# Kernel tuning notes

Hardware: AMD Instinct MI355X
Metric: run time of the kernel (lower is better)

Reference implementation:

```python
import jax, jax.numpy as jnp
import numpy as np

B, P, D, C = 1024, 4, 512, 128  # batch, parts, feat_dim, num_classes


def setup_inputs() -> dict:
    key = jax.random.key(0)
    k1, k2 = jax.random.split(key)
    # scale 0.05 keeps dot products O(1) so exp() stays in fp32 range
    inputs = jax.random.normal(k1, (B, P, D), dtype=jnp.float32) * 0.05
    targets = jax.random.randint(k2, (B,), 0, C, dtype=jnp.int64)
    return {"inputs": inputs, "targets": targets}


def _npairs_loss(inputs, targets):
    b, p, d = inputs.shape
    n = b * p
    X = inputs.reshape(n, d)
    t = jnp.repeat(targets, p)              # (n,) class label per row
    parts = jnp.tile(jnp.arange(p), b)      # (n,) part id per row
    prod = X @ X.T                          # (n, n) similarities

    sc = t[:, None] == t[None, :]           # same class
    sp = parts[:, None] == parts[None, :]   # same attention part
    s_sadc = (~sc) & sp
    s_dasc = sc & (~sp)
    s_dadc = (~sc) & (~sp)

    e_pos = jnp.exp(prod)                   # exp(neg) terms
    e_neg = jnp.exp(-prod)                  # exp(-pos) terms

    def group_loss(pos_mask, neg_mask):
        # sum_i sum_{j in pos_i} log(1 + sum_{k in neg_i} exp(prod[i,k] - prod[i,j]))
        # = sum log1p(S_i * exp(-prod[i,j])) with S_i = sum_{k in neg_i} exp(prod[i,k])
        S = jnp.sum(jnp.where(neg_mask, e_pos, 0.0), axis=1)        # (n,)
        terms = jnp.where(pos_mask, jnp.log1p(S[:, None] * e_neg), 0.0)
        return jnp.sum(terms)

    loss_sadc = group_loss(s_sadc, s_dadc)
    loss_dasc = group_loss(s_dasc, s_dadc)
    # NOTE: original returns loss_sadc twice and never uses loss_sasc (bug kept for fidelity)
    return (loss_sadc + loss_sadc + loss_dasc) / n


def reference(inputs, targets):
    return _npairs_loss(inputs, targets)
```

## Files before the change

### kernel.cpp

```cpp
#include <hip/hip_runtime.h>
#include <stdint.h>

#define GLOBAL_AS __attribute__((address_space(1)))
#define LDS_AS    __attribute__((address_space(3)))

typedef __attribute__((ext_vector_type(8))) __bf16 bf16x8;
typedef __attribute__((ext_vector_type(4))) float  f32x4;

static_assert(sizeof(bf16x8) == 16, "bf16x8 must be 16B");

constexpr int N  = 4096;
constexpr int DK = 512;
constexpr int NTILE = 528;
constexpr int PW = 32;


__global__ void k_convert(const float* __restrict__ X, __bf16* __restrict__ Xb,
                          const int* __restrict__ tbuf, int* __restrict__ cls) {
    if (blockIdx.x == 1024) {
        __shared__ int is64;
        const int t = threadIdx.x;
        if (t == 0) is64 = 1;
        __syncthreads();
        if (tbuf[4 * t + 1] != 0 || tbuf[4 * t + 3] != 0) is64 = 0;
        __syncthreads();
        const int f = is64;
#pragma unroll
        for (int q = 0; q < 4; ++q) {
            const int ti = 4 * t + q;
            const int v = tbuf[f ? 2 * ti : ti];
            cls[4 * ti + 0] = v; cls[4 * ti + 1] = v;
            cls[4 * ti + 2] = v; cls[4 * ti + 3] = v;
        }
        return;
    }
    int idx = blockIdx.x * blockDim.x + threadIdx.x;
    const float4* s = (const float4*)X;
    float4 a = s[2 * idx + 0];
    float4 b = s[2 * idx + 1];
    bf16x8 o;
    o[0] = (__bf16)a.x; o[1] = (__bf16)a.y; o[2] = (__bf16)a.z; o[3] = (__bf16)a.w;
    o[4] = (__bf16)b.x; o[5] = (__bf16)b.y; o[6] = (__bf16)b.z; o[7] = (__bf16)b.w;
    *(bf16x8*)(Xb + 8 * idx) = o;
}

__launch_bounds__(256, 3)
__global__ void k_main(const __bf16* __restrict__ Xb, const int* __restrict__ cls,
                       float* __restrict__ partials) {
    __shared__ __align__(16) char smem[3][16384];
    __shared__ int rowcls[128], colcls[128];
    float4* accR = (float4*)&smem[0][0];
    float4* accC = (float4*)&smem[1][0];

    const int tid  = threadIdx.x;
    const int lane = tid & 63;
    const int wid  = tid >> 6;
    const int wr   = wid >> 1;
    const int wc   = wid & 1;
    const int rA   = lane & 15;
    const int kgrp = lane >> 4;
    const char* xb = (const char*)Xb;

    const int bid = (blockIdx.x & 7) * 66 + (blockIdx.x >> 3);
    int rt = (int)((sqrtf(8.0f * (float)bid + 1.0f) - 1.0f) * 0.5f);
    while (((rt + 1) * (rt + 2)) / 2 <= bid) ++rt;
    while ((rt * (rt + 1)) / 2 > bid) --rt;
    const int g  = bid - (rt * (rt + 1)) / 2;
    const int i0 = rt * 128;
    const int j0 = g * 128;
    const bool offdiag = (rt != g);

    if (tid < 128) rowcls[tid] = cls[i0 + tid];
    else           colcls[tid - 128] = cls[j0 + (tid - 128)];
    __syncthreads();

    size_t gbase[4];
#pragma unroll
    for (int q = 0; q < 4; ++q) {
        const int l    = q * 256 + tid;
        const int prow = l >> 2;
        const int csrc = (l & 3) ^ ((prow >> 1) & 3);
        const int grow = (prow < 128) ? (i0 + prow) : (j0 + prow - 128);
        gbase[q] = (size_t)grow * 1024 + (size_t)(csrc * 16);
    }

#define STAGE(bslot, kt)                                                       \
    {                                                                          \
        char* dst = &smem[(bslot)][0];                                         \
        const size_t kb = (size_t)(kt) * 64;                                   \
        _Pragma("unroll")                                                      \
        for (int q = 0; q < 4; ++q) {                                          \
            __builtin_amdgcn_global_load_lds(                                  \
                (const GLOBAL_AS void*)(xb + gbase[q] + kb),                   \
                (LDS_AS void*)(dst + q * 4096 + wid * 1024), 16, 0, 0);        \
        }                                                                      \
    }

    STAGE(0, 0);
    STAGE(1, 1);

    f32x4 acc[4][4] = {};

#pragma unroll
    for (int t = 0; t < 16; ++t) {
        if (t < 15) { asm volatile("s_waitcnt vmcnt(4)" ::: "memory"); }
        else        { asm volatile("s_waitcnt vmcnt(0)" ::: "memory"); }
        __builtin_amdgcn_s_barrier();
        asm volatile("" ::: "memory");
        if (t + 2 < 16) STAGE((t + 2) % 3, t + 2);
        const char* bp = &smem[t % 3][0];
        bf16x8 af[4], bg[4];
#pragma unroll
        for (int m = 0; m < 4; ++m) {
            const int pr = wr * 64 + m * 16 + rA;
            af[m] = *(const bf16x8*)(bp + pr * 64 + ((kgrp ^ ((pr >> 1) & 3)) << 4));
        }
#pragma unroll
        for (int n = 0; n < 4; ++n) {
            const int pr = 128 + wc * 64 + n * 16 + rA;
            bg[n] = *(const bf16x8*)(bp + pr * 64 + ((kgrp ^ ((pr >> 1) & 3)) << 4));
        }
#pragma unroll
        for (int m = 0; m < 4; ++m)
#pragma unroll
            for (int n = 0; n < 4; ++n)
                acc[m][n] = __builtin_amdgcn_mfma_f32_16x16x32_bf16(bg[n], af[m],
                                                                    acc[m][n], 0, 0, 0);
    }
#undef STAGE

    __syncthreads();

    const int pi = rA & 3;
    int ci[4];
#pragma unroll
    for (int m = 0; m < 4; ++m) ci[m] = rowcls[wr * 64 + m * 16 + rA];
    float rS[4] = {0.f, 0.f, 0.f, 0.f};
    float rP[4] = {0.f, 0.f, 0.f, 0.f};
    float rE[4] = {0.f, 0.f, 0.f, 0.f};
    float rW[4] = {0.f, 0.f, 0.f, 0.f};

#pragma unroll
    for (int n = 0; n < 4; ++n) {
#pragma unroll
        for (int r = 0; r < 4; ++r) {
            const int cj = colcls[wc * 64 + n * 16 + kgrp * 4 + r];
            float cS = 0.f, cP = 0.f, cE = 0.f, cW = 0.f;
#pragma unroll
            for (int m = 0; m < 4; ++m) {
                const float p  = acc[m][n][r];
                const float ep = __expf(p);
                const bool sc = (ci[m] == cj);
                const bool sp = (pi == r);
                if (!sc && !sp) { rS[m] += ep; cS += ep; }
                const float w = (!sc && sp) ? 2.f : ((sc && !sp) ? 1.f : 0.f);
                rP[m] += w * p;  rE[m] += w * ep;  rW[m] += w;
                cP += w * p;     cE += w * ep;     cW += w;
            }
            if (offdiag) {
#pragma unroll
                for (int off = 1; off < 16; off <<= 1) {
                    cS += __shfl_xor(cS, off);
                    cP += __shfl_xor(cP, off);
                    cE += __shfl_xor(cE, off);
                    cW += __shfl_xor(cW, off);
                }
                if (rA == 0)
                    accC[wr * 128 + wc * 64 + n * 16 + kgrp * 4 + r] =
                        make_float4(cS, cP, cE, cW);
            }
        }
    }
#pragma unroll
    for (int m = 0; m < 4; ++m) {
        float vS = rS[m], vP = rP[m], vE = rE[m], vW = rW[m];
        vS += __shfl_xor(vS, 16); vS += __shfl_xor(vS, 32);
        vP += __shfl_xor(vP, 16); vP += __shfl_xor(vP, 32);
        vE += __shfl_xor(vE, 16); vE += __shfl_xor(vE, 32);
        vW += __shfl_xor(vW, 16); vW += __shfl_xor(vW, 32);
        if (kgrp == 0) accR[wc * 128 + wr * 64 + m * 16 + rA] = make_float4(vS, vP, vE, vW);
    }

    __syncthreads();
    if (tid < 128) {
        float4 a0 = accR[tid], a1 = accR[128 + tid];
        ((float4*)partials)[(size_t)(i0 + tid) * PW + g] =
            make_float4(a0.x + a1.x, a0.y + a1.y, a0.z + a1.z, a0.w + a1.w);
    } else if (offdiag) {
        const int c = tid - 128;
        float4 c0 = accC[c], c1 = accC[128 + c];
        ((float4*)partials)[(size_t)(j0 + c) * PW + rt] =
            make_float4(c0.x + c1.x, c0.y + c1.y, c0.z + c1.z, c0.w + c1.w);
    }
}

__global__ void k_rowloss(const float* __restrict__ partials, float* __restrict__ blockSums) {
    __shared__ float red[16];
    const int tid = threadIdx.x;
    const int sub = tid & 15;
    const int row = blockIdx.x * 16 + (tid >> 4);

    const float4* p = ((const float4*)partials) + (size_t)row * PW;
    float4 a = p[sub];
    float4 b = p[sub + 16];
    float S = a.x + b.x, P = a.y + b.y, E = a.z + b.z, W = a.w + b.w;
#pragma unroll
    for (int off = 1; off < 16; off <<= 1) {
        S += __shfl_xor(S, off);
        P += __shfl_xor(P, off);
        E += __shfl_xor(E, off);
        W += __shfl_xor(W, off);
    }
    if (sub == 0) red[tid >> 4] = W * logf(S) - P + E / S;
    __syncthreads();
    if (tid == 0) {
        float s = 0.f;
#pragma unroll
        for (int r = 0; r < 16; ++r) s += red[r];
        blockSums[blockIdx.x] = s;
    }
}

__global__ void k_final2(const float* __restrict__ blockSums, float* __restrict__ out) {
    const int t = threadIdx.x;
    float v = blockSums[t] + blockSums[t + 64] + blockSums[t + 128] + blockSums[t + 192];
#pragma unroll
    for (int off = 1; off < 64; off <<= 1) v += __shfl_xor(v, off);
    if (t == 0) out[0] = v / (float)N;
}

extern "C" void kernel_launch(void* const* d_in, const int* in_sizes, int n_in,
                              void* d_out, int out_size, void* d_ws, size_t ws_size,
                              hipStream_t stream) {
    const float* X = (const float*)d_in[0];
    const int*   T = (const int*)d_in[1];
    float* out = (float*)d_out;

    char* ws = (char*)d_ws;
    __bf16* Xb    = (__bf16*)ws;
    int*    cls   = (int*)(ws + (size_t)4 * 1024 * 1024);
    float*  parts = (float*)(ws + (size_t)4 * 1024 * 1024 + 16 * 1024);
    float*  bsums = (float*)ws;

    hipLaunchKernelGGL(k_convert, dim3(1025),  dim3(256), 0, stream, X, Xb, T, cls);
    hipLaunchKernelGGL(k_main,    dim3(NTILE), dim3(256), 0, stream, Xb, cls, parts);
    hipLaunchKernelGGL(k_rowloss, dim3(256),   dim3(256), 0, stream, parts, bsums);
    hipLaunchKernelGGL(k_final2,  dim3(1),     dim3(64),  0, stream, bsums, out);
}
```

Measured before the change: 57.03 us.

## Switch Gram matrix GEMM from bf16 to fp8 MFMA and transpose partials layout

Inputs are converted to fp8 (e4m3) instead of bf16, halving the bytes staged per row, and the main kernel uses 16x16x32 fp8 MFMAs over 8 K-tiles instead of 16 bf16 tiles. The LDS swizzle and fragment loads are adapted to 8-byte fp8 operands. The partials buffer is transposed to slot-major so the row-loss kernel uses one thread per row with 16 blocks, and the final reduce is shrunk to match. Precision loss from fp8 on the dot products, which feed exp(), may push the loss outside tolerance.

```diff
diff --git a/kernel.cpp b/kernel.cpp
--- a/kernel.cpp
+++ b/kernel.cpp
@@ -4,10 +4,7 @@
 #define GLOBAL_AS __attribute__((address_space(1)))
 #define LDS_AS    __attribute__((address_space(3)))
 
-typedef __attribute__((ext_vector_type(8))) __bf16 bf16x8;
-typedef __attribute__((ext_vector_type(4))) float  f32x4;
-
-static_assert(sizeof(bf16x8) == 16, "bf16x8 must be 16B");
+typedef __attribute__((ext_vector_type(4))) float f32x4;
 
 constexpr int N  = 4096;
 constexpr int DK = 512;
@@ -15,7 +12,7 @@
 constexpr int PW = 32;
 
 
-__global__ void k_convert(const float* __restrict__ X, __bf16* __restrict__ Xb,
+__global__ void k_convert(const float* __restrict__ X, uint32_t* __restrict__ Xb8,
                           const int* __restrict__ tbuf, int* __restrict__ cls) {
     if (blockIdx.x == 1024) {
         __shared__ int is64;
@@ -34,18 +31,21 @@
         }
         return;
     }
-    int idx = blockIdx.x * blockDim.x + threadIdx.x;
+    const int idx = blockIdx.x * blockDim.x + threadIdx.x;
     const float4* s = (const float4*)X;
     float4 a = s[2 * idx + 0];
     float4 b = s[2 * idx + 1];
-    bf16x8 o;
-    o[0] = (__bf16)a.x; o[1] = (__bf16)a.y; o[2] = (__bf16)a.z; o[3] = (__bf16)a.w;
-    o[4] = (__bf16)b.x; o[5] = (__bf16)b.y; o[6] = (__bf16)b.z; o[7] = (__bf16)b.w;
-    *(bf16x8*)(Xb + 8 * idx) = o;
+    uint32_t lo = 0, hi = 0;
+    lo = __builtin_amdgcn_cvt_pk_fp8_f32(a.x, a.y, lo, 0);
+    lo = __builtin_amdgcn_cvt_pk_fp8_f32(a.z, a.w, lo, 1);
+    hi = __builtin_amdgcn_cvt_pk_fp8_f32(b.x, b.y, hi, 0);
+    hi = __builtin_amdgcn_cvt_pk_fp8_f32(b.z, b.w, hi, 1);
+    Xb8[2 * idx + 0] = lo;
+    Xb8[2 * idx + 1] = hi;
 }
 
 __launch_bounds__(256, 3)
-__global__ void k_main(const __bf16* __restrict__ Xb, const int* __restrict__ cls,
+__global__ void k_main(const char* __restrict__ Xb, const int* __restrict__ cls,
                        float* __restrict__ partials) {
     __shared__ __align__(16) char smem[3][16384];
     __shared__ int rowcls[128], colcls[128];
@@ -59,7 +59,6 @@
     const int wc   = wid & 1;
     const int rA   = lane & 15;
     const int kgrp = lane >> 4;
-    const char* xb = (const char*)Xb;
 
     const int bid = (blockIdx.x & 7) * 66 + (blockIdx.x >> 3);
     int rt = (int)((sqrtf(8.0f * (float)bid + 1.0f) - 1.0f) * 0.5f);
@@ -79,9 +78,9 @@
     for (int q = 0; q < 4; ++q) {
         const int l    = q * 256 + tid;
         const int prow = l >> 2;
-        const int csrc = (l & 3) ^ ((prow >> 1) & 3);
+        const int csrc = (l & 3) ^ (prow & 3);
         const int grow = (prow < 128) ? (i0 + prow) : (j0 + prow - 128);
-        gbase[q] = (size_t)grow * 1024 + (size_t)(csrc * 16);
+        gbase[q] = (size_t)grow * DK + (size_t)(csrc * 16);
     }
 
 #define STAGE(bslot, kt)                                                       \
@@ -91,7 +90,7 @@
         _Pragma("unroll")                                                      \
         for (int q = 0; q < 4; ++q) {                                          \
             __builtin_amdgcn_global_load_lds(                                  \
-                (const GLOBAL_AS void*)(xb + gbase[q] + kb),                   \
+                (const GLOBAL_AS void*)(Xb + gbase[q] + kb),                   \
                 (LDS_AS void*)(dst + q * 4096 + wid * 1024), 16, 0, 0);        \
         }                                                                      \
     }
@@ -102,30 +101,35 @@
     f32x4 acc[4][4] = {};
 
 #pragma unroll
-    for (int t = 0; t < 16; ++t) {
-        if (t < 15) { asm volatile("s_waitcnt vmcnt(4)" ::: "memory"); }
-        else        { asm volatile("s_waitcnt vmcnt(0)" ::: "memory"); }
+    for (int t = 0; t < 8; ++t) {
+        if (t < 7) { asm volatile("s_waitcnt vmcnt(4)" ::: "memory"); }
+        else       { asm volatile("s_waitcnt vmcnt(0)" ::: "memory"); }
         __builtin_amdgcn_s_barrier();
         asm volatile("" ::: "memory");
-        if (t + 2 < 16) STAGE((t + 2) % 3, t + 2);
+        if (t + 2 < 8) STAGE((t + 2) % 3, t + 2);
         const char* bp = &smem[t % 3][0];
-        bf16x8 af[4], bg[4];
-#pragma unroll
-        for (int m = 0; m < 4; ++m) {
-            const int pr = wr * 64 + m * 16 + rA;
-            af[m] = *(const bf16x8*)(bp + pr * 64 + ((kgrp ^ ((pr >> 1) & 3)) << 4));
+#pragma unroll
+        for (int kk = 0; kk < 2; ++kk) {
+            long af[4], bg[4];
+            const int c  = kk * 2 + (kgrp >> 1);
+            const int s8 = (kgrp & 1) * 8;
+#pragma unroll
+            for (int m = 0; m < 4; ++m) {
+                const int pr = wr * 64 + m * 16 + rA;
+                af[m] = *(const long*)(bp + pr * 64 + ((c ^ (pr & 3)) << 4) + s8);
+            }
+#pragma unroll
+            for (int n = 0; n < 4; ++n) {
+                const int pr = 128 + wc * 64 + n * 16 + rA;
+                bg[n] = *(const long*)(bp + pr * 64 + ((c ^ (pr & 3)) << 4) + s8);
+            }
+#pragma unroll
+            for (int m = 0; m < 4; ++m)
+#pragma unroll
+                for (int n = 0; n < 4; ++n)
+                    acc[m][n] = __builtin_amdgcn_mfma_f32_16x16x32_fp8_fp8(
+                        bg[n], af[m], acc[m][n], 0, 0, 0);
         }
-#pragma unroll
-        for (int n = 0; n < 4; ++n) {
-            const int pr = 128 + wc * 64 + n * 16 + rA;
-            bg[n] = *(const bf16x8*)(bp + pr * 64 + ((kgrp ^ ((pr >> 1) & 3)) << 4));
-        }
-#pragma unroll
-        for (int m = 0; m < 4; ++m)
-#pragma unroll
-            for (int n = 0; n < 4; ++n)
-                acc[m][n] = __builtin_amdgcn_mfma_f32_16x16x32_bf16(bg[n], af[m],
-                                                                    acc[m][n], 0, 0, 0);
     }
 #undef STAGE
 
@@ -184,48 +188,41 @@
     __syncthreads();
     if (tid < 128) {
         float4 a0 = accR[tid], a1 = accR[128 + tid];
-        ((float4*)partials)[(size_t)(i0 + tid) * PW + g] =
+        ((float4*)partials)[(size_t)g * N + i0 + tid] =
             make_float4(a0.x + a1.x, a0.y + a1.y, a0.z + a1.z, a0.w + a1.w);
     } else if (offdiag) {
         const int c = tid - 128;
         float4 c0 = accC[c], c1 = accC[128 + c];
-        ((float4*)partials)[(size_t)(j0 + c) * PW + rt] =
+        ((float4*)partials)[(size_t)rt * N + j0 + c] =
             make_float4(c0.x + c1.x, c0.y + c1.y, c0.z + c1.z, c0.w + c1.w);
     }
 }
 
 __global__ void k_rowloss(const float* __restrict__ partials, float* __restrict__ blockSums) {
-    __shared__ float red[16];
+    __shared__ float red[256];
     const int tid = threadIdx.x;
-    const int sub = tid & 15;
-    const int row = blockIdx.x * 16 + (tid >> 4);
-
-    const float4* p = ((const float4*)partials) + (size_t)row * PW;
-    float4 a = p[sub];
-    float4 b = p[sub + 16];
-    float S = a.x + b.x, P = a.y + b.y, E = a.z + b.z, W = a.w + b.w;
-#pragma unroll
-    for (int off = 1; off < 16; off <<= 1) {
-        S += __shfl_xor(S, off);
-        P += __shfl_xor(P, off);
-        E += __shfl_xor(E, off);
-        W += __shfl_xor(W, off);
-    }
-    if (sub == 0) red[tid >> 4] = W * logf(S) - P + E / S;
-    __syncthreads();
-    if (tid == 0) {
-        float s = 0.f;
-#pragma unroll
-        for (int r = 0; r < 16; ++r) s += red[r];
-        blockSums[blockIdx.x] = s;
-    }
+    const int row = blockIdx.x * 256 + tid;
+    const float4* p = (const float4*)partials;
+    float S = 0.f, P = 0.f, E = 0.f, W = 0.f;
+#pragma unroll
+    for (int s = 0; s < PW; ++s) {
+        float4 v = p[(size_t)s * N + row];
+        S += v.x; P += v.y; E += v.z; W += v.w;
+    }
+    red[tid] = W * logf(S) - P + E / S;
+    __syncthreads();
+    for (int s = 128; s > 0; s >>= 1) {
+        if (tid < s) red[tid] += red[tid + s];
+        __syncthreads();
+    }
+    if (tid == 0) blockSums[blockIdx.x] = red[0];
 }
 
 __global__ void k_final2(const float* __restrict__ blockSums, float* __restrict__ out) {
     const int t = threadIdx.x;
-    float v = blockSums[t] + blockSums[t + 64] + blockSums[t + 128] + blockSums[t + 192];
-#pragma unroll
-    for (int off = 1; off < 64; off <<= 1) v += __shfl_xor(v, off);
+    float v = (t < 16) ? blockSums[t] : 0.f;
+#pragma unroll
+    for (int off = 1; off < 16; off <<= 1) v += __shfl_xor(v, off);
     if (t == 0) out[0] = v / (float)N;
 }
 
@@ -237,13 +234,14 @@
     float* out = (float*)d_out;
 
     char* ws = (char*)d_ws;
-    __bf16* Xb    = (__bf16*)ws;
-    int*    cls   = (int*)(ws + (size_t)4 * 1024 * 1024);
-    float*  parts = (float*)(ws + (size_t)4 * 1024 * 1024 + 16 * 1024);
-    float*  bsums = (float*)ws;
-
-    hipLaunchKernelGGL(k_convert, dim3(1025),  dim3(256), 0, stream, X, Xb, T, cls);
-    hipLaunchKernelGGL(k_main,    dim3(NTILE), dim3(256), 0, stream, Xb, cls, parts);
-    hipLaunchKernelGGL(k_rowloss, dim3(256),   dim3(256), 0, stream, parts, bsums);
+    char*     Xb8   = ws;
+    int*      cls   = (int*)(ws + (size_t)2 * 1024 * 1024);
+    float*    parts = (float*)(ws + (size_t)2 * 1024 * 1024 + 16 * 1024);
+    float*    bsums = (float*)ws;
+
+    hipLaunchKernelGGL(k_convert, dim3(1025),  dim3(256), 0, stream,
+                       X, (uint32_t*)Xb8, T, cls);
+    hipLaunchKernelGGL(k_main,    dim3(NTILE), dim3(256), 0, stream, Xb8, cls, parts);
+    hipLaunchKernelGGL(k_rowloss, dim3(16),    dim3(256), 0, stream, parts, bsums);
     hipLaunchKernelGGL(k_final2,  dim3(1),     dim3(64),  0, stream, bsums, out);
 }
```

Result: slower. 61.30 us (+7.5%).

## Use 512-thread blocks with 8 waves and double-buffered LDS staging in k_main

Applied to the files above, without the earlier changes.

Doubles the block to 8 wavefronts arranged 2x4, so each wave computes a 64x32 sub-tile instead of 64x64, with correspondingly fewer accumulators per wave. The three-stage LDS ring with explicit vmcnt waits becomes a two-buffer ping-pong synchronised by __syncthreads, and the epilogue reduces four row partials instead of two. The aim is more resident waves to hide latency and lower register pressure. In exchange it gives up prefetch depth and per-wave operand reuse, and the tighter launch-bounds occupancy hint could force register spills.

```diff
diff --git a/kernel.cpp b/kernel.cpp
--- a/kernel.cpp
+++ b/kernel.cpp
@@ -12,7 +12,6 @@
 constexpr int N  = 4096;
 constexpr int DK = 512;
 constexpr int NTILE = 528;
-constexpr int PW = 32;
 
 
 __global__ void k_convert(const float* __restrict__ X, __bf16* __restrict__ Xb,
@@ -44,10 +43,10 @@
     *(bf16x8*)(Xb + 8 * idx) = o;
 }
 
-__launch_bounds__(256, 3)
+__launch_bounds__(512, 6)
 __global__ void k_main(const __bf16* __restrict__ Xb, const int* __restrict__ cls,
                        float* __restrict__ partials) {
-    __shared__ __align__(16) char smem[3][16384];
+    __shared__ __align__(16) char smem[2][16384];
     __shared__ int rowcls[128], colcls[128];
     float4* accR = (float4*)&smem[0][0];
     float4* accC = (float4*)&smem[1][0];
@@ -55,8 +54,8 @@
     const int tid  = threadIdx.x;
     const int lane = tid & 63;
     const int wid  = tid >> 6;
-    const int wr   = wid >> 1;
-    const int wc   = wid & 1;
+    const int wr   = wid >> 2;
+    const int wc   = wid & 3;
     const int rA   = lane & 15;
     const int kgrp = lane >> 4;
     const char* xb = (const char*)Xb;
@@ -70,62 +69,63 @@
     const int j0 = g * 128;
     const bool offdiag = (rt != g);
 
-    if (tid < 128) rowcls[tid] = cls[i0 + tid];
-    else           colcls[tid - 128] = cls[j0 + (tid - 128)];
-    __syncthreads();
-
-    size_t gbase[4];
-#pragma unroll
-    for (int q = 0; q < 4; ++q) {
-        const int l    = q * 256 + tid;
+    if (tid < 128) {
+        rowcls[tid] = cls[i0 + tid];
+        colcls[tid] = cls[j0 + tid];
+    }
+
+    size_t gbase[2];
+#pragma unroll
+    for (int q = 0; q < 2; ++q) {
+        const int l    = q * 512 + tid;
         const int prow = l >> 2;
         const int csrc = (l & 3) ^ ((prow >> 1) & 3);
         const int grow = (prow < 128) ? (i0 + prow) : (j0 + prow - 128);
         gbase[q] = (size_t)grow * 1024 + (size_t)(csrc * 16);
     }
 
-#define STAGE(bslot, kt)                                                       \
+#define STAGE(buf, kt)                                                         \
     {                                                                          \
-        char* dst = &smem[(bslot)][0];                                         \
+        char* dst = &smem[(buf)][0];                                           \
         const size_t kb = (size_t)(kt) * 64;                                   \
         _Pragma("unroll")                                                      \
-        for (int q = 0; q < 4; ++q) {                                          \
+        for (int q = 0; q < 2; ++q) {                                          \
             __builtin_amdgcn_global_load_lds(                                  \
                 (const GLOBAL_AS void*)(xb + gbase[q] + kb),                   \
-                (LDS_AS void*)(dst + q * 4096 + wid * 1024), 16, 0, 0);        \
+                (LDS_AS void*)(dst + q * 8192 + tid * 16), 16, 0, 0);          \
         }                                                                      \
     }
 
     STAGE(0, 0);
-    STAGE(1, 1);
-
-    f32x4 acc[4][4] = {};
-
-#pragma unroll
-    for (int t = 0; t < 16; ++t) {
-        if (t < 15) { asm volatile("s_waitcnt vmcnt(4)" ::: "memory"); }
-        else        { asm volatile("s_waitcnt vmcnt(0)" ::: "memory"); }
-        __builtin_amdgcn_s_barrier();
-        asm volatile("" ::: "memory");
-        if (t + 2 < 16) STAGE((t + 2) % 3, t + 2);
-        const char* bp = &smem[t % 3][0];
-        bf16x8 af[4], bg[4];
+    __syncthreads();
+
+    f32x4 acc[4][2] = {};
+    int cur = 0;
+#pragma unroll
+    for (int kt = 0; kt < 16; ++kt) {
+        if (kt < 15) STAGE(cur ^ 1, kt + 1);
+        const char* bp = &smem[cur][0];
+        bf16x8 af[4], bg[2];
 #pragma unroll
         for (int m = 0; m < 4; ++m) {
             const int pr = wr * 64 + m * 16 + rA;
             af[m] = *(const bf16x8*)(bp + pr * 64 + ((kgrp ^ ((pr >> 1) & 3)) << 4));
         }
 #pragma unroll
-        for (int n = 0; n < 4; ++n) {
-            const int pr = 128 + wc * 64 + n * 16 + rA;
+        for (int n = 0; n < 2; ++n) {
+            const int pr = 128 + wc * 32 + n * 16 + rA;
             bg[n] = *(const bf16x8*)(bp + pr * 64 + ((kgrp ^ ((pr >> 1) & 3)) << 4));
         }
 #pragma unroll
         for (int m = 0; m < 4; ++m)
 #pragma unroll
-            for (int n = 0; n < 4; ++n)
+            for (int n = 0; n < 2; ++n)
                 acc[m][n] = __builtin_amdgcn_mfma_f32_16x16x32_bf16(bg[n], af[m],
                                                                     acc[m][n], 0, 0, 0);
+        if (kt < 15) {
+            __syncthreads();
+            cur ^= 1;
+        }
     }
 #undef STAGE
 
@@ -135,16 +135,17 @@
     int ci[4];
 #pragma unroll
     for (int m = 0; m < 4; ++m) ci[m] = rowcls[wr * 64 + m * 16 + rA];
+
     float rS[4] = {0.f, 0.f, 0.f, 0.f};
     float rP[4] = {0.f, 0.f, 0.f, 0.f};
     float rE[4] = {0.f, 0.f, 0.f, 0.f};
     float rW[4] = {0.f, 0.f, 0.f, 0.f};
 
 #pragma unroll
-    for (int n = 0; n < 4; ++n) {
+    for (int n = 0; n < 2; ++n) {
 #pragma unroll
         for (int r = 0; r < 4; ++r) {
-            const int cj = colcls[wc * 64 + n * 16 + kgrp * 4 + r];
+            const int cj = colcls[wc * 32 + n * 16 + kgrp * 4 + r];
             float cS = 0.f, cP = 0.f, cE = 0.f, cW = 0.f;
 #pragma unroll
             for (int m = 0; m < 4; ++m) {
@@ -166,7 +167,7 @@
                     cW += __shfl_xor(cW, off);
                 }
                 if (rA == 0)
-                    accC[wr * 128 + wc * 64 + n * 16 + kgrp * 4 + r] =
+                    accC[wr * 128 + wc * 32 + n * 16 + kgrp * 4 + r] =
                         make_float4(cS, cP, cE, cW);
             }
         }
@@ -178,19 +179,22 @@
         vP += __shfl_xor(vP, 16); vP += __shfl_xor(vP, 32);
         vE += __shfl_xor(vE, 16); vE += __shfl_xor(vE, 32);
         vW += __shfl_xor(vW, 16); vW += __shfl_xor(vW, 32);
-        if (kgrp == 0) accR[wc * 128 + wr * 64 + m * 16 + rA] = make_float4(vS, vP, vE, vW);
+        if (kgrp == 0)
+            accR[wc * 128 + wr * 64 + m * 16 + rA] = make_float4(vS, vP, vE, vW);
     }
 
     __syncthreads();
     if (tid < 128) {
-        float4 a0 = accR[tid], a1 = accR[128 + tid];
-        ((float4*)partials)[(size_t)(i0 + tid) * PW + g] =
-            make_float4(a0.x + a1.x, a0.y + a1.y, a0.z + a1.z, a0.w + a1.w);
-    } else if (offdiag) {
-        const int c = tid - 128;
-        float4 c0 = accC[c], c1 = accC[128 + c];
-        ((float4*)partials)[(size_t)(j0 + c) * PW + rt] =
-            make_float4(c0.x + c1.x, c0.y + c1.y, c0.z + c1.z, c0.w + c1.w);
+        float4 a0 = accR[tid],       a1 = accR[128 + tid];
+        float4 a2 = accR[256 + tid], a3 = accR[384 + tid];
+        ((float4*)partials)[(size_t)(i0 + tid) * 32 + g] =
+            make_float4(a0.x + a1.x + a2.x + a3.x, a0.y + a1.y + a2.y + a3.y,
+                        a0.z + a1.z + a2.z + a3.z, a0.w + a1.w + a2.w + a3.w);
+        if (offdiag) {
+            float4 c0 = accC[tid], c1 = accC[128 + tid];
+            ((float4*)partials)[(size_t)(j0 + tid) * 32 + rt] =
+                make_float4(c0.x + c1.x, c0.y + c1.y, c0.z + c1.z, c0.w + c1.w);
+        }
     }
 }
 
@@ -200,7 +204,7 @@
     const int sub = tid & 15;
     const int row = blockIdx.x * 16 + (tid >> 4);
 
-    const float4* p = ((const float4*)partials) + (size_t)row * PW;
+    const float4* p = ((const float4*)partials) + (size_t)row * 32;
     float4 a = p[sub];
     float4 b = p[sub + 16];
     float S = a.x + b.x, P = a.y + b.y, E = a.z + b.z, W = a.w + b.w;
@@ -243,7 +247,7 @@
     float*  bsums = (float*)ws;
 
     hipLaunchKernelGGL(k_convert, dim3(1025),  dim3(256), 0, stream, X, Xb, T, cls);
-    hipLaunchKernelGGL(k_main,    dim3(NTILE), dim3(256), 0, stream, Xb, cls, parts);
+    hipLaunchKernelGGL(k_main,    dim3(NTILE), dim3(512), 0, stream, Xb, cls, parts);
     hipLaunchKernelGGL(k_rowloss, dim3(256),   dim3(256), 0, stream, parts, bsums);
     hipLaunchKernelGGL(k_final2,  dim3(1),     dim3(64),  0, stream, bsums, out);
 }
```

Result: faster. 54.42 us (-4.6%).
